# Optimization experiments

Measured on AMD Instinct MI355X. Metric: run time of the kernel, lower is better.

Reference implementation:

```python
import jax, jax.numpy as jnp
import numpy as np


def setup_inputs() -> dict:
    key = jax.random.key(0)
    ks = jax.random.split(key, 10)
    B, L, D_MODEL = 2, 2048, 1024
    D_INNER, N, W, R = 2048, 16, 4, 64
    s = 0.02
    return {
        "hidden_states": jax.random.normal(ks[0], (B, L, D_MODEL), jnp.float32),
        "in_proj_w": jax.random.normal(ks[1], (2 * D_INNER, D_MODEL), jnp.float32) * s,
        "conv_w": jax.random.normal(ks[2], (D_INNER, W), jnp.float32) * 0.2,
        "conv_b": jax.random.normal(ks[3], (D_INNER,), jnp.float32) * 0.02,
        "x_proj_w": jax.random.normal(ks[4], (R + 2 * N, D_INNER), jnp.float32) * s,
        "dt_proj_w": jax.random.normal(ks[5], (D_INNER, R), jnp.float32) * (R ** -0.5),
        "dt_proj_b": jnp.log(jnp.expm1(jnp.exp(jax.random.uniform(ks[6], (D_INNER,), jnp.float32, np.log(1e-3), np.log(1e-1)))) + 1e-20),
        "A_log": jnp.log(jnp.broadcast_to(jnp.arange(1, N + 1, dtype=jnp.float32), (D_INNER, N))),
        "D_param": jnp.ones((D_INNER,), jnp.float32),
        "out_proj_w": jax.random.normal(ks[7], (D_MODEL, D_INNER), jnp.float32) * s,
    }


def _mamba_fwd(hidden_states, in_proj_w, conv_w, conv_b, x_proj_w,
               dt_proj_w, dt_proj_b, A_log, D_param, out_proj_w):
    Bsz, L, _ = hidden_states.shape
    d_inner = conv_w.shape[0]
    n = A_log.shape[1]
    r = dt_proj_w.shape[1]

    # input projection -> x, z  (each [B, L, d_inner])
    xz = jnp.einsum('bld,ed->ble', hidden_states, in_proj_w)
    x, z = xz[..., :d_inner], xz[..., d_inner:]

    # depthwise causal conv over L with SiLU
    x_bdl = jnp.transpose(x, (0, 2, 1))  # [B, d, L]
    kern = conv_w[:, None, :]            # [d, 1, W]
    xc = jax.lax.conv_general_dilated(
        x_bdl, kern, window_strides=(1,), padding=[(conv_w.shape[1] - 1, 0)],
        dimension_numbers=('NCH', 'OIH', 'NCH'), feature_group_count=d_inner)
    xc = xc + conv_b[None, :, None]
    xc = xc * jax.nn.sigmoid(xc)         # silu, [B, d, L]
    u = jnp.transpose(xc, (0, 2, 1))     # [B, L, d]

    # SSM parameter projections
    x_dbl = jnp.einsum('bld,ed->ble', u, x_proj_w)   # [B, L, r+2n]
    dt_lo = x_dbl[..., :r]
    B_ssm = x_dbl[..., r:r + n]                       # [B, L, n]
    C_ssm = x_dbl[..., r + n:]                        # [B, L, n]
    delta = jax.nn.softplus(jnp.einsum('blr,dr->bld', dt_lo, dt_proj_w) + dt_proj_b)

    A = -jnp.exp(A_log)  # [d, n]

    # selective scan over time (sequential recurrence)
    def step(h, inp):
        d_t, u_t, b_t, c_t = inp  # [B,d], [B,d], [B,n], [B,n]
        dA = jnp.exp(d_t[..., None] * A)                       # [B,d,n]
        h = dA * h + (d_t * u_t)[..., None] * b_t[:, None, :]  # [B,d,n]
        y_t = jnp.einsum('bdn,bn->bd', h, c_t)
        return h, y_t

    h0 = jnp.zeros((Bsz, d_inner, n), dtype=u.dtype)
    xs = (jnp.transpose(delta, (1, 0, 2)), jnp.transpose(u, (1, 0, 2)),
          jnp.transpose(B_ssm, (1, 0, 2)), jnp.transpose(C_ssm, (1, 0, 2)))
    _, ys = jax.lax.scan(step, h0, xs)           # ys: [L, B, d]
    y = jnp.transpose(ys, (1, 0, 2)) + u * D_param
    y = y * (z * jax.nn.sigmoid(z))              # gate: y * silu(z)
    return jnp.einsum('bld,ed->ble', y, out_proj_w)


def reference(hidden_states, in_proj_w, conv_w, conv_b, x_proj_w,
              dt_proj_w, dt_proj_b, A_log, D_param, out_proj_w):
    return _mamba_fwd(hidden_states, in_proj_w, conv_w, conv_b, x_proj_w,
                      dt_proj_w, dt_proj_b, A_log, D_param, out_proj_w)
```

## Files before the change

kernel.cpp:

```cpp
#include <hip/hip_runtime.h>
#include <cstdint>
#include <cstddef>

#define Bsz  2
#define Lseq 2048
#define DM   1024
#define DI   2048
#define NS   16
#define RR   64
#define BL   (Bsz * Lseq)
#define TC   64
#define NC   (Lseq / TC)

typedef unsigned short u16;
typedef __attribute__((ext_vector_type(4))) unsigned short u16x4;
typedef __attribute__((ext_vector_type(8))) short short8;
typedef __attribute__((ext_vector_type(4))) float f32x4;

__device__ __forceinline__ u16 f32_to_bf16(float f) {
  union { float f; unsigned int u; } v; v.f = f;
  unsigned int lsb = (v.u >> 16) & 1u;
  v.u += 0x7fffu + lsb;
  return (u16)(v.u >> 16);
}
__device__ __forceinline__ float bf16_to_f32(u16 h) {
  union { unsigned int u; float f; } v; v.u = ((unsigned int)h) << 16;
  return v.f;
}

__global__ void cvt_f32_bf16(const float* __restrict__ src, u16* __restrict__ dst, int n) {
  int i = (blockIdx.x * blockDim.x + threadIdx.x) * 4;
  if (i + 4 <= n) {
    float4 v = *(const float4*)(src + i);
    dst[i + 0] = f32_to_bf16(v.x);
    dst[i + 1] = f32_to_bf16(v.y);
    dst[i + 2] = f32_to_bf16(v.z);
    dst[i + 3] = f32_to_bf16(v.w);
  } else {
    for (; i < n; ++i) dst[i] = f32_to_bf16(src[i]);
  }
}

__global__ void split_bf16_kernel(const float* __restrict__ src,
                                  u16* __restrict__ hi, u16* __restrict__ lo, int n) {
  int i = blockIdx.x * blockDim.x + threadIdx.x;
  if (i >= n) return;
  const float v = src[i];
  const u16 h = f32_to_bf16(v);
  hi[i] = h;
  lo[i] = f32_to_bf16(v - bf16_to_f32(h));
}

__device__ __forceinline__ void gload_lds16(const u16* g, u16* l) {
  __builtin_amdgcn_global_load_lds(
      (const __attribute__((address_space(1))) unsigned int*)g,
      (__attribute__((address_space(3))) unsigned int*)l,
      16, 0, 0);
}

template<bool BF16OUT>
__global__ __launch_bounds__(256) void gemm128_bt(
    const u16* __restrict__ A, const u16* __restrict__ Bt,
    void* __restrict__ outA_, void* __restrict__ outB_,
    int split, int ldA, int ldB, int K)
{
  __shared__ __align__(16) u16 As[128 * 32];
  __shared__ __align__(16) u16 Bs[128 * 32];
  const int tid  = threadIdx.x;
  const int lane = tid & 63;
  const int wid  = tid >> 6;
  const int m0 = blockIdx.y * 128;
  const int n0 = blockIdx.x * 128;
  const int wr = wid >> 1, wc = wid & 1;

  const f32x4 zero = {0.f, 0.f, 0.f, 0.f};
  f32x4 acc[4][4];
#pragma unroll
  for (int i = 0; i < 4; ++i)
#pragma unroll
    for (int j = 0; j < 4; ++j) acc[i][j] = zero;

  const int l16 = lane * 16;

  for (int k0 = 0; k0 < K; k0 += 32) {
    __syncthreads();
#pragma unroll
    for (int c = 0; c < 2; ++c) {
      const int base = c * 4096 + wid * 1024;
      const int ofs  = base + l16;
      const int row  = ofs >> 6;
      const int col  = (ofs >> 1) & 31;
      gload_lds16(A  + (size_t)(m0 + row) * K + k0 + col, (u16*)((char*)As + base));
      gload_lds16(Bt + (size_t)(n0 + row) * K + k0 + col, (u16*)((char*)Bs + base));
    }
    __syncthreads();

    const int kk = (lane >> 4) * 8;
    const int ra = wr * 64 + (lane & 15);
    const int rb = wc * 64 + (lane & 15);
    short8 af[4], bf[4];
#pragma unroll
    for (int i = 0; i < 4; ++i) af[i] = *(const short8*)&As[(ra + i * 16) * 32 + kk];
#pragma unroll
    for (int j = 0; j < 4; ++j) bf[j] = *(const short8*)&Bs[(rb + j * 16) * 32 + kk];
#pragma unroll
    for (int i = 0; i < 4; ++i)
#pragma unroll
      for (int j = 0; j < 4; ++j)
        acc[i][j] = __builtin_amdgcn_mfma_f32_16x16x32_bf16(af[i], bf[j], acc[i][j], 0, 0, 0);
  }

  const int cr = (lane >> 4) * 4;
  const int cc = lane & 15;
#pragma unroll
  for (int i = 0; i < 4; ++i)
#pragma unroll
    for (int j = 0; j < 4; ++j)
#pragma unroll
      for (int r = 0; r < 4; ++r) {
        const int m = m0 + wr * 64 + i * 16 + cr + r;
        const int n = n0 + wc * 64 + j * 16 + cc;
        const float v = acc[i][j][r];
        const bool isA = (n < split);
        const int  nn  = isA ? n : n - split;
        const int  ld  = isA ? ldA : ldB;
        if constexpr (BF16OUT) {
          u16* o = isA ? (u16*)outA_ : (u16*)outB_;
          o[(size_t)m * ld + nn] = f32_to_bf16(v);
        } else {
          float* o = isA ? (float*)outA_ : (float*)outB_;
          o[(size_t)m * ld + nn] = v;
        }
      }
}

__global__ __launch_bounds__(256) void gemm_xproj(
    const u16* __restrict__ A, const u16* __restrict__ Bt,
    float* __restrict__ xdbl, u16* __restrict__ dhi, u16* __restrict__ dlo)
{
  const int wg   = blockIdx.x * 4 + (threadIdx.x >> 6);
  const int lane = threadIdx.x & 63;
  const int mt = wg / 6, nt = wg % 6;

  const u16* arow = A  + (size_t)(mt * 16 + (lane & 15)) * DI + ((lane >> 4) * 8);
  const u16* brow = Bt + (size_t)(nt * 16 + (lane & 15)) * DI + ((lane >> 4) * 8);
  f32x4 acc = {0.f, 0.f, 0.f, 0.f};
  for (int k0 = 0; k0 < DI; k0 += 32) {
    short8 a = *(const short8*)(arow + k0);
    short8 b = *(const short8*)(brow + k0);
    acc = __builtin_amdgcn_mfma_f32_16x16x32_bf16(a, b, acc, 0, 0, 0);
  }
  const int cr = (lane >> 4) * 4, cc = lane & 15;
  const int n  = nt * 16 + cc;
#pragma unroll
  for (int r = 0; r < 4; ++r) {
    const int m = mt * 16 + cr + r;
    const float v = acc[r];
    if (n < RR) {
      const u16 h = f32_to_bf16(v);
      dhi[(size_t)m * RR + n] = h;
      dlo[(size_t)m * RR + n] = f32_to_bf16(v - bf16_to_f32(h));
    } else {
      xdbl[(size_t)m * 96 + n] = v;
    }
  }
}

__global__ __launch_bounds__(256) void dt_gemm_mfma(
    const u16* __restrict__ ahi, const u16* __restrict__ alo,
    const u16* __restrict__ bhi, const u16* __restrict__ blo,
    const float* __restrict__ dtb, float* __restrict__ delta)
{
  const int wg   = blockIdx.x * 4 + (threadIdx.x >> 6);
  const int lane = threadIdx.x & 63;
  const int mt = wg >> 7, nt = wg & 127;

  const size_t aofs = (size_t)(mt * 16 + (lane & 15)) * 64 + ((lane >> 4) * 8);
  const size_t bofs = (size_t)(nt * 16 + (lane & 15)) * 64 + ((lane >> 4) * 8);

  f32x4 acc = {0.f, 0.f, 0.f, 0.f};
#pragma unroll
  for (int k0 = 0; k0 < 64; k0 += 32) {
    const short8 Ah = *(const short8*)(ahi + aofs + k0);
    const short8 Al = *(const short8*)(alo + aofs + k0);
    const short8 Bh = *(const short8*)(bhi + bofs + k0);
    const short8 Bl = *(const short8*)(blo + bofs + k0);
    acc = __builtin_amdgcn_mfma_f32_16x16x32_bf16(Ah, Bh, acc, 0, 0, 0);
    acc = __builtin_amdgcn_mfma_f32_16x16x32_bf16(Ah, Bl, acc, 0, 0, 0);
    acc = __builtin_amdgcn_mfma_f32_16x16x32_bf16(Al, Bh, acc, 0, 0, 0);
  }

  const int cr = (lane >> 4) * 4, cc = lane & 15;
  const int n  = nt * 16 + cc;
  const float b = dtb[n];
#pragma unroll
  for (int r = 0; r < 4; ++r) {
    const float s = acc[r] + b;
    const float sp = fmaxf(s, 0.f) + __logf(1.f + __expf(-fabsf(s)));
    delta[(size_t)(mt * 16 + cr + r) * DI + n] = sp;
  }
}

__global__ void conv_silu_kernel(const u16* __restrict__ x,
                                 const float* __restrict__ cw, const float* __restrict__ cb,
                                 u16* __restrict__ ub)
{
  const int idx  = blockIdx.x * blockDim.x + threadIdx.x;
  const int base = idx * 4;
  const int d  = base & (DI - 1);
  const int bl = base >> 11;
  const int l  = bl & (Lseq - 1);
  const u16* xp = x + (size_t)bl * DI + d;
  const u16x4 zv = {0, 0, 0, 0};
  const u16x4 x3 = *(const u16x4*)xp;
  const u16x4 x2 = (l >= 1) ? *(const u16x4*)(xp - DI)     : zv;
  const u16x4 x1 = (l >= 2) ? *(const u16x4*)(xp - 2 * DI) : zv;
  const u16x4 x0 = (l >= 3) ? *(const u16x4*)(xp - 3 * DI) : zv;
  const float4 bias = *(const float4*)&cb[d];
  u16x4 out;
#pragma unroll
  for (int j = 0; j < 4; ++j) {
    const float4 w = *(const float4*)&cw[(d + j) * 4];
    float acc = ((const float*)&bias)[j];
    acc += bf16_to_f32(x0[j]) * w.x + bf16_to_f32(x1[j]) * w.y +
           bf16_to_f32(x2[j]) * w.z + bf16_to_f32(x3[j]) * w.w;
    const float s = acc / (1.f + __expf(-acc));
    out[j] = f32_to_bf16(s);
  }
  *(u16x4*)(ub + (size_t)bl * DI + d) = out;
}


__global__ __launch_bounds__(256) void scan_chunk_ps(
    const float* __restrict__ delta, const u16* __restrict__ u,
    const float* __restrict__ xdbl, const float* __restrict__ alog,
    float* __restrict__ Pout, float* __restrict__ Sout)
{
  __shared__ float Bl[TC][NS];
  const int b   = blockIdx.z;
  const int c   = blockIdx.y;
  const int d   = blockIdx.x * 256 + threadIdx.x;
  const int tid = threadIdx.x;
  const size_t rowBase = (size_t)b * Lseq + (size_t)c * TC;

  {
    const int row = tid >> 2, c4 = (tid & 3) * 4;
    *(float4*)&Bl[row][c4] = *(const float4*)&xdbl[(rowBase + row) * 96 + RR + c4];
  }
  __syncthreads();

  float A[NS];
#pragma unroll
  for (int n4 = 0; n4 < 4; ++n4) {
    const float4 a4 = *(const float4*)&alog[(size_t)d * NS + n4 * 4];
    A[n4 * 4 + 0] = -__expf(a4.x);
    A[n4 * 4 + 1] = -__expf(a4.y);
    A[n4 * 4 + 2] = -__expf(a4.z);
    A[n4 * 4 + 3] = -__expf(a4.w);
  }

  float h[NS], P[NS];
#pragma unroll
  for (int n = 0; n < NS; ++n) { h[n] = 0.f; P[n] = 1.f; }

#pragma unroll 4
  for (int t = 0; t < TC; ++t) {
    const float dt  = delta[(rowBase + t) * DI + d];
    const float ut  = bf16_to_f32(u[(rowBase + t) * DI + d]);
    const float dtu = dt * ut;
#pragma unroll
    for (int n = 0; n < NS; ++n) {
      const float dA = __expf(dt * A[n]);
      P[n] *= dA;
      h[n] = dA * h[n] + dtu * Bl[t][n];
    }
  }

  const size_t base = (size_t)(b * NC + c) * NS * DI + d;
#pragma unroll
  for (int n = 0; n < NS; ++n) {
    Pout[base + (size_t)n * DI] = P[n];
    Sout[base + (size_t)n * DI] = h[n];
  }
}

__global__ __launch_bounds__(256) void scan_combine(
    const float* __restrict__ P, const float* __restrict__ S,
    float* __restrict__ Hin)
{
  const int gid = blockIdx.x * 256 + threadIdx.x;
  const int b   = gid >> 15;
  const int nd  = gid & 32767;
  float h = 0.f;
  for (int c = 0; c < NC; ++c) {
    const size_t o = (size_t)(b * NC + c) * (NS * DI) + nd;
    const float Pc = P[o];
    const float Sc = S[o];
    Hin[o] = h;
    h = Pc * h + Sc;
  }
}

__global__ __launch_bounds__(256) void scan_chunk_y(
    const float* __restrict__ delta, const u16* __restrict__ u,
    const float* __restrict__ xdbl, const float* __restrict__ alog,
    const float* __restrict__ dpar, const u16* __restrict__ z,
    const float* __restrict__ Hin, u16* __restrict__ yb)
{
  __shared__ float Bl[TC][NS];
  __shared__ float Cl[TC][NS];
  const int b   = blockIdx.z;
  const int c   = blockIdx.y;
  const int d   = blockIdx.x * 256 + threadIdx.x;
  const int tid = threadIdx.x;
  const size_t rowBase = (size_t)b * Lseq + (size_t)c * TC;

  {
    const int row = tid >> 2, c4 = (tid & 3) * 4;
    *(float4*)&Bl[row][c4] = *(const float4*)&xdbl[(rowBase + row) * 96 + RR + c4];
    *(float4*)&Cl[row][c4] = *(const float4*)&xdbl[(rowBase + row) * 96 + RR + NS + c4];
  }
  __syncthreads();

  float A[NS];
#pragma unroll
  for (int n4 = 0; n4 < 4; ++n4) {
    const float4 a4 = *(const float4*)&alog[(size_t)d * NS + n4 * 4];
    A[n4 * 4 + 0] = -__expf(a4.x);
    A[n4 * 4 + 1] = -__expf(a4.y);
    A[n4 * 4 + 2] = -__expf(a4.z);
    A[n4 * 4 + 3] = -__expf(a4.w);
  }
  const float Dv = dpar[d];

  float h[NS];
  const size_t sbase = (size_t)(b * NC + c) * NS * DI + d;
#pragma unroll
  for (int n = 0; n < NS; ++n) h[n] = Hin[sbase + (size_t)n * DI];

#pragma unroll 4
  for (int t = 0; t < TC; ++t) {
    const float dt  = delta[(rowBase + t) * DI + d];
    const float ut  = bf16_to_f32(u[(rowBase + t) * DI + d]);
    const float zv  = bf16_to_f32(z[(rowBase + t) * DI + d]);
    const float dtu = dt * ut;
    float y = 0.f;
#pragma unroll
    for (int n = 0; n < NS; ++n) {
      const float dA = __expf(dt * A[n]);
      h[n] = dA * h[n] + dtu * Bl[t][n];
      y += h[n] * Cl[t][n];
    }
    const float yv = y + ut * Dv;
    const float g  = zv / (1.f + __expf(-zv));
    yb[(rowBase + t) * DI + d] = f32_to_bf16(yv * g);
  }
}

extern "C" void kernel_launch(void* const* d_in, const int* in_sizes, int n_in,
                              void* d_out, int out_size, void* d_ws, size_t ws_size,
                              hipStream_t stream)
{
  const float* hs   = (const float*)d_in[0];
  const float* win  = (const float*)d_in[1];
  const float* cw   = (const float*)d_in[2];
  const float* cb   = (const float*)d_in[3];
  const float* wxp  = (const float*)d_in[4];
  const float* wdt  = (const float*)d_in[5];
  const float* bdt  = (const float*)d_in[6];
  const float* alog = (const float*)d_in[7];
  const float* dpar = (const float*)d_in[8];
  const float* wout = (const float*)d_in[9];
  float* out = (float*)d_out;

  char* ws = (char*)d_ws;
  size_t off = 0;
  auto alloc = [&](size_t bytes) -> void* {
    void* p = ws + off;
    off += (bytes + 255) & ~(size_t)255;
    return p;
  };
  u16*   hs_b   = (u16*)  alloc((size_t)BL * DM * 2);
  u16*   win_b  = (u16*)  alloc((size_t)2 * DI * DM * 2);
  u16*   wxp_b  = (u16*)  alloc((size_t)96 * DI * 2);
  u16*   wout_b = (u16*)  alloc((size_t)DM * DI * 2);
  u16*   xbuf   = (u16*)  alloc((size_t)BL * DI * 2);
  u16*   zbuf   = (u16*)  alloc((size_t)BL * DI * 2);
  u16*   ub16   = (u16*)  alloc((size_t)BL * DI * 2);
  float* deltab = (float*)alloc((size_t)BL * DI * 4);
  float* xdbl   = (float*)alloc((size_t)BL * 96 * 4);
  float* Pbuf   = (float*)alloc((size_t)Bsz * NC * DI * NS * 4);
  float* Sbuf   = (float*)alloc((size_t)Bsz * NC * DI * NS * 4);
  u16*   dt_hi  = (u16*)  alloc((size_t)BL * 64 * 2);
  u16*   dt_lo  = (u16*)  alloc((size_t)BL * 64 * 2);
  u16*   w_hi   = (u16*)  alloc((size_t)DI * 64 * 2);
  u16*   w_lo   = (u16*)  alloc((size_t)DI * 64 * 2);
  u16*   y_b    = ub16;
  float* Hin    = Pbuf;

  const int thr = 256;
  cvt_f32_bf16<<<(BL * DM / 4 + thr - 1) / thr, thr, 0, stream>>>(hs, hs_b, BL * DM);
  cvt_f32_bf16<<<(2 * DI * DM / 4 + thr - 1) / thr, thr, 0, stream>>>(win, win_b, 2 * DI * DM);
  cvt_f32_bf16<<<(96 * DI / 4 + thr - 1) / thr, thr, 0, stream>>>(wxp, wxp_b, 96 * DI);
  cvt_f32_bf16<<<(DM * DI / 4 + thr - 1) / thr, thr, 0, stream>>>(wout, wout_b, DM * DI);
  split_bf16_kernel<<<(DI * 64) / thr, thr, 0, stream>>>(wdt, w_hi, w_lo, DI * 64);

  {
    dim3 g(4096 / 128, BL / 128);
    gemm128_bt<true><<<g, 256, 0, stream>>>(hs_b, win_b, xbuf, zbuf, DI, DI, DI, DM);
  }

  conv_silu_kernel<<<(BL * DI / 4) / 256, 256, 0, stream>>>(xbuf, cw, cb, ub16);

  gemm_xproj<<<(256 * 6) / 4, 256, 0, stream>>>(ub16, wxp_b, xdbl, dt_hi, dt_lo);

  dt_gemm_mfma<<<(256 * 128) / 4, 256, 0, stream>>>(dt_hi, dt_lo, w_hi, w_lo, bdt, deltab);

  {
    dim3 gA(DI / 256, NC, Bsz);
    scan_chunk_ps<<<gA, 256, 0, stream>>>(deltab, ub16, xdbl, alog, Pbuf, Sbuf);
    scan_combine<<<(Bsz * DI * NS) / 256, 256, 0, stream>>>(Pbuf, Sbuf, Hin);
    scan_chunk_y<<<gA, 256, 0, stream>>>(deltab, ub16, xdbl, alog, dpar, zbuf, Hin, y_b);
  }

  {
    dim3 g(DM / 128, BL / 128);
    gemm128_bt<false><<<g, 256, 0, stream>>>(y_b, wout_b, out, out, DM, DM, DM, DI);
  }
}
```

Measured before the change: 294.1 us.

## Split-K out_proj GEMM, remap workgroups across XCDs, hoist epilogue branch

The out_proj GEMM is now split along K into two halves using a z grid dimension. Each half writes fp32 partial results into the reused delta buffer, and a new add kernel sums them. This doubles the number of workgroups for a grid that previously had only 256 tiles. Both GEMMs also remap block ids so consecutive tiles are spread across the 8 XCDs, and the epilogue's per-element split check moves outside the loops. In exchange the change adds an extra partial-sum write and read plus one more kernel launch.

Result: no change. 291.8 us (-0.8%).

```diff
diff --git a/kernel.cpp b/kernel.cpp
--- a/kernel.cpp
+++ b/kernel.cpp
@@ -62,15 +62,21 @@
 __global__ __launch_bounds__(256) void gemm128_bt(
     const u16* __restrict__ A, const u16* __restrict__ Bt,
     void* __restrict__ outA_, void* __restrict__ outB_,
-    int split, int ldA, int ldB, int K)
+    int split, int ldA, int ldB, int K, int kstride, size_t zstride)
 {
   __shared__ __align__(16) u16 As[128 * 32];
   __shared__ __align__(16) u16 Bs[128 * 32];
   const int tid  = threadIdx.x;
   const int lane = tid & 63;
   const int wid  = tid >> 6;
-  const int m0 = blockIdx.y * 128;
-  const int n0 = blockIdx.x * 128;
+
+  const int nwg = gridDim.x * gridDim.y;
+  int wg = blockIdx.y * gridDim.x + blockIdx.x;
+  wg = (wg & 7) * (nwg >> 3) + (wg >> 3);
+  const int m0 = (wg / gridDim.x) * 128;
+  const int n0 = (wg % gridDim.x) * 128;
+  const int kbase = blockIdx.z * K;
+
   const int wr = wid >> 1, wc = wid & 1;
 
   const f32x4 zero = {0.f, 0.f, 0.f, 0.f};
@@ -90,8 +96,8 @@
       const int ofs  = base + l16;
       const int row  = ofs >> 6;
       const int col  = (ofs >> 1) & 31;
-      gload_lds16(A  + (size_t)(m0 + row) * K + k0 + col, (u16*)((char*)As + base));
-      gload_lds16(Bt + (size_t)(n0 + row) * K + k0 + col, (u16*)((char*)Bs + base));
+      gload_lds16(A  + (size_t)(m0 + row) * kstride + kbase + k0 + col, (u16*)((char*)As + base));
+      gload_lds16(Bt + (size_t)(n0 + row) * kstride + kbase + k0 + col, (u16*)((char*)Bs + base));
     }
     __syncthreads();
 
@@ -110,28 +116,45 @@
         acc[i][j] = __builtin_amdgcn_mfma_f32_16x16x32_bf16(af[i], bf[j], acc[i][j], 0, 0, 0);
   }
 
+  const bool isA = (n0 < split);
+  const int  ld  = isA ? ldA : ldB;
+  const int  nb  = isA ? n0 : n0 - split;
   const int cr = (lane >> 4) * 4;
   const int cc = lane & 15;
-#pragma unroll
-  for (int i = 0; i < 4; ++i)
-#pragma unroll
-    for (int j = 0; j < 4; ++j)
-#pragma unroll
-      for (int r = 0; r < 4; ++r) {
-        const int m = m0 + wr * 64 + i * 16 + cr + r;
-        const int n = n0 + wc * 64 + j * 16 + cc;
-        const float v = acc[i][j][r];
-        const bool isA = (n < split);
-        const int  nn  = isA ? n : n - split;
-        const int  ld  = isA ? ldA : ldB;
-        if constexpr (BF16OUT) {
-          u16* o = isA ? (u16*)outA_ : (u16*)outB_;
-          o[(size_t)m * ld + nn] = f32_to_bf16(v);
-        } else {
-          float* o = isA ? (float*)outA_ : (float*)outB_;
-          o[(size_t)m * ld + nn] = v;
+  if constexpr (BF16OUT) {
+    u16* o = (u16*)(isA ? outA_ : outB_);
+#pragma unroll
+    for (int i = 0; i < 4; ++i)
+#pragma unroll
+      for (int j = 0; j < 4; ++j)
+#pragma unroll
+        for (int r = 0; r < 4; ++r) {
+          const int m = m0 + wr * 64 + i * 16 + cr + r;
+          const int n = nb + wc * 64 + j * 16 + cc;
+          o[(size_t)m * ld + n] = f32_to_bf16(acc[i][j][r]);
         }
-      }
+  } else {
+    float* o = (float*)(isA ? outA_ : outB_) + (size_t)blockIdx.z * zstride;
+#pragma unroll
+    for (int i = 0; i < 4; ++i)
+#pragma unroll
+      for (int j = 0; j < 4; ++j)
+#pragma unroll
+        for (int r = 0; r < 4; ++r) {
+          const int m = m0 + wr * 64 + i * 16 + cr + r;
+          const int n = nb + wc * 64 + j * 16 + cc;
+          o[(size_t)m * ld + n] = acc[i][j][r];
+        }
+  }
+}
+
+__global__ void add2_kernel(const float* __restrict__ part, float* __restrict__ out) {
+  const int i = (blockIdx.x * blockDim.x + threadIdx.x) * 4;
+  const float4 a = *(const float4*)(part + i);
+  const float4 b = *(const float4*)(part + (size_t)BL * DM + i);
+  float4 s;
+  s.x = a.x + b.x; s.y = a.y + b.y; s.z = a.z + b.z; s.w = a.w + b.w;
+  *(float4*)(out + i) = s;
 }
 
 __global__ __launch_bounds__(256) void gemm_xproj(
@@ -397,6 +420,7 @@
   u16*   w_lo   = (u16*)  alloc((size_t)DI * 64 * 2);
   u16*   y_b    = ub16;
   float* Hin    = Pbuf;
+  float* part   = deltab;
 
   const int thr = 256;
   cvt_f32_bf16<<<(BL * DM / 4 + thr - 1) / thr, thr, 0, stream>>>(hs, hs_b, BL * DM);
@@ -407,7 +431,8 @@
 
   {
     dim3 g(4096 / 128, BL / 128);
-    gemm128_bt<true><<<g, 256, 0, stream>>>(hs_b, win_b, xbuf, zbuf, DI, DI, DI, DM);
+    gemm128_bt<true><<<g, 256, 0, stream>>>(hs_b, win_b, xbuf, zbuf,
+                                            DI, DI, DI, DM, DM, 0);
   }
 
   conv_silu_kernel<<<(BL * DI / 4) / 256, 256, 0, stream>>>(xbuf, cw, cb, ub16);
@@ -424,7 +449,10 @@
   }
 
   {
-    dim3 g(DM / 128, BL / 128);
-    gemm128_bt<false><<<g, 256, 0, stream>>>(y_b, wout_b, out, out, DM, DM, DM, DI);
-  }
-}
+    dim3 g(DM / 128, BL / 128, 2);
+    gemm128_bt<false><<<g, 256, 0, stream>>>(y_b, wout_b, part, part,
+                                             1 << 30, DM, DM, DI / 2, DI,
+                                             (size_t)BL * DM);
+    add2_kernel<<<(BL * DM / 4) / 256, 256, 0, stream>>>(part, out);
+  }
+}
```
